# Kernel optimization log

Measured on AMD Instinct MI355X. Metric: run time of the kernel, lower is better.

The kernel has to match this reference:

```python
import jax, jax.numpy as jnp
import numpy as np

B, F, T = 4, 2048, 2048
CF, CT = 1024, 1024
H, DH = 16, 64
ALPHA = 1.0 / np.sqrt(DH).astype(np.float32)


def setup_inputs() -> dict:
    key = jax.random.key(0)
    ks = jax.random.split(key, 8)
    s = 0.02  # trunc_normal-ish init scale
    return {
        "from_tensor": jax.random.normal(ks[0], (B, F, CF), jnp.float32),
        "to_tensor": jax.random.normal(ks[1], (B, T, CT), jnp.float32),
        "mask": jax.random.randint(ks[2], (B, F, T), 0, 2, jnp.int32),
        "Wq": jax.random.normal(ks[3], (CF, H * DH), jnp.float32) * s,
        "bq": jnp.zeros((H * DH,), jnp.float32),
        "Wk": jax.random.normal(ks[4], (CT, H * DH), jnp.float32) * s,
        "bk": jnp.zeros((H * DH,), jnp.float32),
        "Wv": jax.random.normal(ks[5], (CT, H * DH), jnp.float32) * s,
        "bv": jnp.zeros((H * DH,), jnp.float32),
    }


def reference(from_tensor, to_tensor, mask, Wq, bq, Wk, bk, Wv, bv):
    # projections (nn.Linear with no activation)
    q = from_tensor @ Wq + bq          # [B,F,H*DH]
    k = to_tensor @ Wk + bk            # [B,T,H*DH]
    v = to_tensor @ Wv + bv            # [B,T,H*DH]
    q = q.reshape(B, F, H, DH)         # query: [..., F, H, DH]
    k = k.reshape(B, T, DH, H)         # key:   [..., T, DH, H]  (self._shape[::-1])
    v = v.reshape(B, T, H, DH)
    # score = transpose(q,-3,-2) @ transpose(k,-3,-1) * alpha -> [B,H,F,T]
    score = jnp.einsum("bfhd,btdh->bhft", q, k) * ALPHA
    if mask is not None:
        adder = (1.0 - mask[:, None].astype(score.dtype)) * -100000.0  # [B,1,F,T]
        score = score + adder
    probs = jax.nn.softmax(score, axis=-1)  # dropout p=0.0 -> identity
    # context = probs @ transpose(v,-3,-2), then transpose back: [B,F,H,DH]
    context = jnp.einsum("bhft,bthd->bfhd", probs, v)
    return context.reshape(B, F, H * DH)
```

## Files before the change

### kernel.cpp

```cpp
#include <hip/hip_runtime.h>
#include <type_traits>

typedef __bf16 bf16_t;
typedef __attribute__((ext_vector_type(8))) __bf16 bf16x8;
typedef __attribute__((ext_vector_type(4))) float f32x4;
typedef __attribute__((ext_vector_type(16))) float f32x16;

__device__ __forceinline__ void async16(const void* g, void* lds) {
  __builtin_amdgcn_global_load_lds((const __attribute__((address_space(1))) unsigned int*)g,
                                   (__attribute__((address_space(3))) unsigned int*)lds, 16, 0, 0);
}

__device__ __forceinline__ unsigned pk2(float lo, float hi) {
  unsigned short a = __builtin_bit_cast(unsigned short, (__bf16)lo);
  unsigned short b = __builtin_bit_cast(unsigned short, (__bf16)hi);
  return (unsigned)a | ((unsigned)b << 16);
}

__device__ __forceinline__ void plswap(unsigned& a, unsigned& b) {
#if __has_builtin(__builtin_amdgcn_permlane32_swap)
  auto r = __builtin_amdgcn_permlane32_swap((int)a, (int)b, false, false);
  a = (unsigned)r[0];
  b = (unsigned)r[1];
#else
  const bool hb = (threadIdx.x & 32) != 0;
  unsigned bx = (unsigned)__shfl_xor((int)b, 32);
  unsigned ax = (unsigned)__shfl_xor((int)a, 32);
  unsigned na = hb ? bx : a;
  unsigned nb = hb ? b : ax;
  a = na; b = nb;
#endif
}

__global__ __launch_bounds__(256) void pack_mask_kernel(const int* __restrict__ mask,
                                                        unsigned long long* __restrict__ mb) {
  const int lane = threadIdx.x & 63, w = threadIdx.x >> 6;
  for (int i = 0; i < 32; ++i) {
    size_t word = (size_t)blockIdx.x * 128 + (size_t)i * 4 + w;
    unsigned long long bits = __ballot(mask[word * 64 + lane] != 0);
    if (lane == 0) mb[word] = bits;
  }
}

__global__ __launch_bounds__(256) void cvt_bf16_kernel(const float* __restrict__ in, bf16_t* __restrict__ out) {
  size_t i = (size_t)blockIdx.x * 256 + threadIdx.x;
  const float4* in4 = (const float4*)in;
  float4 a = in4[i * 2], b = in4[i * 2 + 1];
  bf16x8 o;
  o[0] = (__bf16)a.x; o[1] = (__bf16)a.y; o[2] = (__bf16)a.z; o[3] = (__bf16)a.w;
  o[4] = (__bf16)b.x; o[5] = (__bf16)b.y; o[6] = (__bf16)b.z; o[7] = (__bf16)b.w;
  *(bf16x8*)(out + i * 8) = o;
}

__global__ __launch_bounds__(256) void wt_cvt_kernel(const float* __restrict__ Wq, const float* __restrict__ Wk,
                                                     const float* __restrict__ Wv, bf16_t* __restrict__ Wt) {
  const int z = blockIdx.z;
  const float* src = (z == 0) ? Wq : ((z == 1) ? Wk : Wv);
  const float sc = (z == 0) ? 0.18033688011112042f : 1.0f;
  bf16_t* dst = Wt + (size_t)z * 1024 * 1024;
  const int n = blockIdx.x * 64 + (threadIdx.x & 63);
  const int k8 = blockIdx.y * 4 + (threadIdx.x >> 6);
  bf16x8 o;
#pragma unroll
  for (int j = 0; j < 8; ++j) o[j] = (__bf16)(src[(size_t)(k8 * 8 + j) * 1024 + n] * sc);
  *(bf16x8*)(dst + (size_t)n * 1024 + k8 * 8) = o;
}

__global__ __launch_bounds__(256) void proj_kernel(const bf16_t* __restrict__ A, const bf16_t* __restrict__ Wt,
                                                   const float* __restrict__ bias, bf16_t* __restrict__ dst,
                                                   const int z, const float bscale) {
  __shared__ __align__(16) unsigned char smem[33792];
  bf16_t* se = (bf16_t*)smem;
  const int tid = threadIdx.x, lane = tid & 63, w = tid >> 6;
  const int m0 = blockIdx.x * 128, n0 = blockIdx.y * 128;
  const int wm = (w >> 1) * 64, wn = (w & 1) * 64;
  const int r = lane & 15, kq = lane >> 4;
  const int srow = lane >> 2, sslot = lane & 3;
  f32x4 acc[4][4] = {};

  auto stage = [&](int buf, int k0) {
    bf16_t* Ad = se + buf * 4096;
    bf16_t* Bd = se + 8192 + buf * 4096;
#pragma unroll
    for (int it = 0; it < 2; ++it) {
      const int c = it * 4 + w;
      const int row = c * 16 + srow;
      async16(A + (size_t)(m0 + row) * 1024 + k0 + ((sslot ^ (row & 3)) * 8), Ad + c * 512);
      async16(Wt + (size_t)(n0 + row) * 1024 + k0 + ((sslot ^ (row & 3)) * 8), Bd + c * 512);
    }
  };

  stage(0, 0);
  __syncthreads();
  for (int tile = 0; tile < 32; ++tile) {
    const int cur = tile & 1;
    if (tile < 31) stage(cur ^ 1, (tile + 1) * 32);
    const bf16_t* Al = se + cur * 4096;
    const bf16_t* Bl = se + 8192 + cur * 4096;
    bf16x8 af[4], bfr[4];
#pragma unroll
    for (int i = 0; i < 4; ++i) {
      const int ra = wm + i * 16 + r;
      af[i] = *(const bf16x8*)(Al + ra * 32 + ((kq ^ (ra & 3)) * 8));
      const int rb = wn + i * 16 + r;
      bfr[i] = *(const bf16x8*)(Bl + rb * 32 + ((kq ^ (rb & 3)) * 8));
    }
    __builtin_amdgcn_s_setprio(1);
#pragma unroll
    for (int i = 0; i < 4; ++i)
#pragma unroll
      for (int j = 0; j < 4; ++j)
        acc[i][j] = __builtin_amdgcn_mfma_f32_16x16x32_bf16(af[i], bfr[j], acc[i][j], 0, 0, 0);
    __builtin_amdgcn_s_setprio(0);
    __syncthreads();
  }

  bf16_t* Cl = se;
  float bvv[4];
#pragma unroll
  for (int j = 0; j < 4; ++j) bvv[j] = bias[n0 + wn + j * 16 + r] * bscale;
#pragma unroll
  for (int i = 0; i < 4; ++i)
#pragma unroll
    for (int j = 0; j < 4; ++j)
#pragma unroll
      for (int g = 0; g < 4; ++g)
        Cl[(wm + i * 16 + kq * 4 + g) * 132 + wn + j * 16 + r] = (__bf16)(acc[i][j][g] + bvv[j]);
  __syncthreads();

  const int b = m0 >> 11, sbase = m0 & 2047;
  if (z == 0) {
#pragma unroll
    for (int q = 0; q < 8; ++q) {
      const int cid = q * 256 + tid;
      const int m = cid >> 4, c = (cid >> 3) & 1, d8 = cid & 7;
      bf16x8 val = *(const bf16x8*)(Cl + m * 132 + c * 64 + d8 * 8);
      *(bf16x8*)(dst + ((size_t)(b * 16 + (n0 >> 6) + c) * 2048 + sbase + m) * 64 + d8 * 8) = val;
    }
  } else if (z == 1) {
#pragma unroll
    for (int q = 0; q < 8; ++q) {
      const int cid = q * 256 + tid;
      const int hh = cid >> 7, m = cid & 127;
      bf16x8 val;
#pragma unroll
      for (int dd = 0; dd < 8; ++dd) val[dd] = Cl[m * 132 + dd * 16 + hh];
      *(bf16x8*)(dst + ((size_t)(b * 16 + hh) * 2048 + sbase + m) * 64 + (n0 >> 4)) = val;
    }
  } else {
#pragma unroll
    for (int q = 0; q < 8; ++q) {
      const int cid = q * 256 + tid;
      const int nl = cid >> 4, m8 = cid & 15;
      bf16x8 val;
#pragma unroll
      for (int s = 0; s < 8; ++s) val[s] = Cl[(m8 * 8 + s) * 132 + nl];
      const int hh = (n0 >> 6) + (nl >> 6), dd = nl & 63;
      *(bf16x8*)(dst + ((size_t)(b * 16 + hh) * 64 + dd) * 2048 + sbase + m8 * 8) = val;
    }
  }
}

__global__ __launch_bounds__(256, 2) void attn_kernel(const bf16_t* __restrict__ Q, const bf16_t* __restrict__ K,
                                                      const bf16_t* __restrict__ VT,
                                                      const unsigned long long* __restrict__ mb,
                                                      float* __restrict__ out) {
  __shared__ __align__(16) unsigned char smem[32768];
  bf16_t* se = (bf16_t*)smem;
  const int tid = threadIdx.x, lane = tid & 63, w = tid >> 6;
  const int cl = lane & 31, hi = lane >> 5;
  const int f0 = blockIdx.x * 256, h = blockIdx.y, b = blockIdx.z;
  const size_t bh = (size_t)b * 16 + h;
  const int fw = f0 + w * 64;

  const bf16_t* Qb = Q + (bh * 2048 + fw) * 64;
  bf16x8 qf[2][4];
#pragma unroll
  for (int fb = 0; fb < 2; ++fb)
#pragma unroll
    for (int ks = 0; ks < 4; ++ks)
      qf[fb][ks] = *(const bf16x8*)(Qb + (fb * 32 + cl) * 64 + ks * 16 + hi * 8);

  f32x16 Of[2][2] = {};
  float lacc[2] = {0.f, 0.f};
  bf16x8 paw[2][4];

  const unsigned long long* mrow[2];
  mrow[0] = mb + ((size_t)b * 2048 + fw + cl) * 32;
  mrow[1] = mb + ((size_t)b * 2048 + fw + 32 + cl) * 32;

  const int row8 = lane >> 3, slot = lane & 7;
  const int swz = (slot ^ row8) * 8;
  const bf16_t* kgb[2];
  const bf16_t* vgb[2];
#pragma unroll
  for (int it = 0; it < 2; ++it) {
    const int row = it * 32 + w * 8 + row8;
    kgb[it] = K + (bh * 2048 + row) * 64 + swz;
    vgb[it] = VT + (bh * 64 + row) * 2048 + swz;
  }

  auto stage_k = [&](int buf, int tile) {
    bf16_t* kd = se + buf * 4096 + w * 512;
#pragma unroll
    for (int it = 0; it < 2; ++it)
      async16(kgb[it] + (size_t)tile * 4096, kd + it * 2048);
  };
  auto stage_v = [&](int buf, int tile) {
    bf16_t* vd = se + 8192 + buf * 4096 + w * 512;
#pragma unroll
    for (int it = 0; it < 2; ++it)
      async16(vgb[it] + (size_t)tile * 64, vd + it * 2048);
  };

  auto pv_step = [&](int vbuf) {
    const bf16_t* Vl = se + 8192 + vbuf * 4096;
    __builtin_amdgcn_s_setprio(1);
#pragma unroll
    for (int db = 0; db < 2; ++db) {
      const int vrow0 = db * 32 + cl;
#pragma unroll
      for (int kt = 0; kt < 4; ++kt) {
        bf16x8 vf = *(const bf16x8*)(Vl + vrow0 * 64 + (((2 * kt + hi) ^ (vrow0 & 7)) * 8));
        Of[0][db] = __builtin_amdgcn_mfma_f32_32x32x16_bf16(paw[0][kt], vf, Of[0][db], 0, 0, 0);
        Of[1][db] = __builtin_amdgcn_mfma_f32_32x32x16_bf16(paw[1][kt], vf, Of[1][db], 0, 0, 0);
      }
    }
    __builtin_amdgcn_s_setprio(0);
  };

  unsigned long long mA[2], mB[2];
  stage_k(0, 0);
  mA[0] = mrow[0][0];
  mA[1] = mrow[1][0];
  __syncthreads();

  auto body = [&](auto curc, auto dopvc, unsigned long long (&mc)[2], unsigned long long (&mn)[2], int tile) {
    constexpr int cur = decltype(curc)::value;
    constexpr bool dopv = decltype(dopvc)::value;
    if (tile < 31) {
      stage_k(cur ^ 1, tile + 1);
      mn[0] = mrow[0][tile + 1];
      mn[1] = mrow[1][tile + 1];
    }
    stage_v(cur, tile);
    const bf16_t* Kl = se + cur * 4096;

    f32x16 st0[2] = {};
    {
      const int krow = cl;
      __builtin_amdgcn_s_setprio(1);
#pragma unroll
      for (int ks = 0; ks < 4; ++ks) {
        bf16x8 kf = *(const bf16x8*)(Kl + krow * 64 + (((2 * ks + hi) ^ (krow & 7)) * 8));
        st0[0] = __builtin_amdgcn_mfma_f32_32x32x16_bf16(kf, qf[0][ks], st0[0], 0, 0, 0);
        st0[1] = __builtin_amdgcn_mfma_f32_32x32x16_bf16(kf, qf[1][ks], st0[1], 0, 0, 0);
      }
      __builtin_amdgcn_s_setprio(0);
    }

    if constexpr (dopv) pv_step(cur ^ 1);

    f32x16 st1[2] = {};
    {
      const int krow = 32 + cl;
      __builtin_amdgcn_s_setprio(1);
#pragma unroll
      for (int ks = 0; ks < 4; ++ks) {
        bf16x8 kf = *(const bf16x8*)(Kl + krow * 64 + (((2 * ks + hi) ^ (krow & 7)) * 8));
        st1[0] = __builtin_amdgcn_mfma_f32_32x32x16_bf16(kf, qf[0][ks], st1[0], 0, 0, 0);
        st1[1] = __builtin_amdgcn_mfma_f32_32x32x16_bf16(kf, qf[1][ks], st1[1], 0, 0, 0);
      }
      __builtin_amdgcn_s_setprio(0);
    }

#pragma unroll
    for (int ts = 0; ts < 2; ++ts) {
#pragma unroll
      for (int fb = 0; fb < 2; ++fb) {
        const f32x16& stf = (ts == 0) ? st0[fb] : st1[fb];
        const unsigned mword = (unsigned)(mc[fb] >> (ts * 32 + 4 * hi));
        float pv[16];
#pragma unroll
        for (int q = 0; q < 4; ++q)
#pragma unroll
          for (int e = 0; e < 4; ++e) {
            const int idx = q * 4 + e;
            float p = __builtin_amdgcn_exp2f(stf[idx]);
            p = ((mword >> (e + 8 * q)) & 1u) ? p : 0.f;
            lacc[fb] += p;
            pv[idx] = p;
          }
#pragma unroll
        for (int kl = 0; kl < 2; ++kl) {
          const int qa = 2 * kl, qb = qa + 1;
          unsigned x0 = pk2(pv[qa * 4 + 0], pv[qa * 4 + 1]);
          unsigned y0 = pk2(pv[qb * 4 + 0], pv[qb * 4 + 1]);
          unsigned x1 = pk2(pv[qa * 4 + 2], pv[qa * 4 + 3]);
          unsigned y1 = pk2(pv[qb * 4 + 2], pv[qb * 4 + 3]);
          plswap(x0, y0);
          plswap(x1, y1);
          union { unsigned u[4]; bf16x8 v; } tmp;
          tmp.u[0] = x0; tmp.u[1] = x1; tmp.u[2] = y0; tmp.u[3] = y1;
          paw[fb][ts * 2 + kl] = tmp.v;
        }
      }
    }
    __syncthreads();
  };

  using c0 = std::integral_constant<int, 0>;
  using c1 = std::integral_constant<int, 1>;
  using bF = std::integral_constant<bool, false>;
  using bT = std::integral_constant<bool, true>;

  body(c0{}, bF{}, mA, mB, 0);
  body(c1{}, bT{}, mB, mA, 1);
  for (int tile = 2; tile < 32; tile += 2) {
    body(c0{}, bT{}, mA, mB, tile);
    body(c1{}, bT{}, mB, mA, tile + 1);
  }
  pv_step(1);

#pragma unroll
  for (int fb = 0; fb < 2; ++fb) lacc[fb] += __shfl_xor(lacc[fb], 32);
  float* lsh = (float*)smem;
  if (hi == 0) {
    lsh[w * 64 + cl] = lacc[0];
    lsh[w * 64 + 32 + cl] = lacc[1];
  }
#pragma unroll
  for (int fb = 0; fb < 2; ++fb)
#pragma unroll
    for (int q = 0; q < 4; ++q)
#pragma unroll
      for (int e = 0; e < 4; ++e) {
        const int idx = q * 4 + e;
        const int row = e + 8 * q + 4 * hi;
        const float li = 1.0f / lsh[w * 64 + fb * 32 + row];
        const size_t orow = ((size_t)b * 2048 + fw + fb * 32 + row) * 1024 + h * 64;
        out[orow + cl] = Of[fb][0][idx] * li;
        out[orow + 32 + cl] = Of[fb][1][idx] * li;
      }
}

extern "C" void kernel_launch(void* const* d_in, const int* in_sizes, int n_in,
                              void* d_out, int out_size, void* d_ws, size_t ws_size,
                              hipStream_t stream) {
  (void)in_sizes; (void)n_in; (void)out_size; (void)ws_size;
  const float* from = (const float*)d_in[0];
  const float* to_  = (const float*)d_in[1];
  const int*   mask = (const int*)d_in[2];
  const float* Wq = (const float*)d_in[3];
  const float* bq = (const float*)d_in[4];
  const float* Wk = (const float*)d_in[5];
  const float* bk = (const float*)d_in[6];
  const float* Wv = (const float*)d_in[7];
  const float* bv = (const float*)d_in[8];
  float* out = (float*)d_out;
  char* ws = (char*)d_ws;

  bf16_t* Qw = (bf16_t*)(ws);
  bf16_t* Kw = (bf16_t*)(ws + (size_t)(1u << 24));
  bf16_t* Vw = (bf16_t*)(ws + (size_t)(2u << 24));
  bf16_t* Wt = (bf16_t*)(ws + (size_t)(3u << 24));
  unsigned long long* mbits = (unsigned long long*)(ws + (size_t)(3u << 24) + (size_t)(6u << 20));
  bf16_t* inb = (bf16_t*)(ws + (size_t)(3u << 24) + (size_t)(8u << 20));

  pack_mask_kernel<<<2048, 256, 0, stream>>>(mask, mbits);
  wt_cvt_kernel<<<dim3(16, 32, 3), 256, 0, stream>>>(Wq, Wk, Wv, Wt);
  cvt_bf16_kernel<<<4096, 256, 0, stream>>>(from, inb);
  proj_kernel<<<dim3(64, 8), 256, 0, stream>>>(inb, Wt, bq, Qw, 0, 0.18033688011112042f);
  cvt_bf16_kernel<<<4096, 256, 0, stream>>>(to_, inb);
  proj_kernel<<<dim3(64, 8), 256, 0, stream>>>(inb, Wt + (1u << 20), bk, Kw, 1, 1.0f);
  proj_kernel<<<dim3(64, 8), 256, 0, stream>>>(inb, Wt + (2u << 20), bv, Vw, 2, 1.0f);
  attn_kernel<<<dim3(8, 16, 4), 256, 0, stream>>>(Qw, Kw, Vw, mbits, out);
}
```

Before: 225.3 us.

## Fold mask into score accumulator init and compute row sums via MFMA

Instead of selecting on mask bits after exp2, the score accumulators are now initialised with a large negative bias (-30000) where masked and zero otherwise, so exp2 drives masked entries to zero. The per-row softmax denominator is computed by MFMAs multiplying the bf16 probabilities by a ones vector, rather than by scalar adds plus a shuffle and LDS reduction. This removes VALU select/add work and the end-of-kernel reduction, at the cost of extra MFMAs per tile, bf16-rounded denominators, and 32 more accumulator registers.

```diff
diff --git a/kernel.cpp b/kernel.cpp
--- a/kernel.cpp
+++ b/kernel.cpp
@@ -181,8 +181,12 @@
     for (int ks = 0; ks < 4; ++ks)
       qf[fb][ks] = *(const bf16x8*)(Qb + (fb * 32 + cl) * 64 + ks * 16 + hi * 8);
 
+  bf16x8 ones8;
+#pragma unroll
+  for (int j = 0; j < 8; ++j) ones8[j] = (__bf16)1.0f;
+
   f32x16 Of[2][2] = {};
-  float lacc[2] = {0.f, 0.f};
+  f32x16 Ol[2] = {};
   bf16x8 paw[2][4];
 
   const unsigned long long* mrow[2];
@@ -246,7 +250,22 @@
     stage_v(cur, tile);
     const bf16_t* Kl = se + cur * 4096;
 
-    f32x16 st0[2] = {};
+    f32x16 st0[2], st1[2];
+#pragma unroll
+    for (int fb = 0; fb < 2; ++fb) {
+      const unsigned mw0 = ~((unsigned)(mc[fb] >> (4 * hi)));
+      const unsigned mw1 = ~((unsigned)(mc[fb] >> (32 + 4 * hi)));
+#pragma unroll
+      for (int q = 0; q < 4; ++q)
+#pragma unroll
+        for (int e = 0; e < 4; ++e) {
+          const int idx = q * 4 + e;
+          const int pos = e + 8 * q;
+          st0[fb][idx] = __uint_as_float(((unsigned)(((int)(mw0 << (31 - pos))) >> 31)) & 0xC6EA6000u);
+          st1[fb][idx] = __uint_as_float(((unsigned)(((int)(mw1 << (31 - pos))) >> 31)) & 0xC6EA6000u);
+        }
+    }
+
     {
       const int krow = cl;
       __builtin_amdgcn_s_setprio(1);
@@ -261,7 +280,6 @@
 
     if constexpr (dopv) pv_step(cur ^ 1);
 
-    f32x16 st1[2] = {};
     {
       const int krow = 32 + cl;
       __builtin_amdgcn_s_setprio(1);
@@ -279,17 +297,13 @@
 #pragma unroll
       for (int fb = 0; fb < 2; ++fb) {
         const f32x16& stf = (ts == 0) ? st0[fb] : st1[fb];
-        const unsigned mword = (unsigned)(mc[fb] >> (ts * 32 + 4 * hi));
         float pv[16];
 #pragma unroll
         for (int q = 0; q < 4; ++q)
 #pragma unroll
           for (int e = 0; e < 4; ++e) {
             const int idx = q * 4 + e;
-            float p = __builtin_amdgcn_exp2f(stf[idx]);
-            p = ((mword >> (e + 8 * q)) & 1u) ? p : 0.f;
-            lacc[fb] += p;
-            pv[idx] = p;
+            pv[idx] = __builtin_amdgcn_exp2f(stf[idx]);
           }
 #pragma unroll
         for (int kl = 0; kl < 2; ++kl) {
@@ -306,6 +320,14 @@
         }
       }
     }
+
+    __builtin_amdgcn_s_setprio(1);
+#pragma unroll
+    for (int kt = 0; kt < 4; ++kt) {
+      Ol[0] = __builtin_amdgcn_mfma_f32_32x32x16_bf16(paw[0][kt], ones8, Ol[0], 0, 0, 0);
+      Ol[1] = __builtin_amdgcn_mfma_f32_32x32x16_bf16(paw[1][kt], ones8, Ol[1], 0, 0, 0);
+    }
+    __builtin_amdgcn_s_setprio(0);
     __syncthreads();
   };
 
@@ -323,13 +345,6 @@
   pv_step(1);
 
 #pragma unroll
-  for (int fb = 0; fb < 2; ++fb) lacc[fb] += __shfl_xor(lacc[fb], 32);
-  float* lsh = (float*)smem;
-  if (hi == 0) {
-    lsh[w * 64 + cl] = lacc[0];
-    lsh[w * 64 + 32 + cl] = lacc[1];
-  }
-#pragma unroll
   for (int fb = 0; fb < 2; ++fb)
 #pragma unroll
     for (int q = 0; q < 4; ++q)
@@ -337,7 +352,7 @@
       for (int e = 0; e < 4; ++e) {
         const int idx = q * 4 + e;
         const int row = e + 8 * q + 4 * hi;
-        const float li = 1.0f / lsh[w * 64 + fb * 32 + row];
+        const float li = 1.0f / Ol[fb][idx];
         const size_t orow = ((size_t)b * 2048 + fw + fb * 32 + row) * 1024 + h * 64;
         out[orow + cl] = Of[fb][0][idx] * li;
         out[orow + 32 + cl] = Of[fb][1][idx] * li;
```

Result: slower. 301.8 us (+34.0%).
